# Kernel tuning notes

Hardware: AMD Instinct MI355X
Metric: run time of the kernel (lower is better)

The kernel has to match this reference:

```python
import jax, jax.numpy as jnp
import numpy as np

B, L, D, H = 2, 2048, 2048, 16
HD = D // H           # head_dim = 128
HD2 = HD // 2         # rotary pair count = 64


def setup_inputs() -> dict:
    key = jax.random.key(0)
    ks = jax.random.split(key, 6)
    x = jax.random.normal(ks[0], (B, L, D), dtype=jnp.float32)
    # RoPE angles: theta_i = 10000^(-2i/HD), angles[l, i] = l * theta_i
    inv_freq = 1.0 / (10000.0 ** (np.arange(0, HD, 2, dtype=np.float32) / HD))
    angles = np.arange(L, dtype=np.float32)[:, None] * inv_freq[None, :]  # [L, HD2]
    freqs_cos = jnp.asarray(np.cos(angles))[None]  # [1, L, HD2]
    freqs_sin = jnp.asarray(np.sin(angles))[None]  # [1, L, HD2]
    s = 1.0 / np.sqrt(D)
    Wq = jax.random.normal(ks[1], (D, D), dtype=jnp.float32) * s
    Wk = jax.random.normal(ks[2], (D, D), dtype=jnp.float32) * s
    Wv = jax.random.normal(ks[3], (D, D), dtype=jnp.float32) * s
    Wo = jax.random.normal(ks[4], (D, D), dtype=jnp.float32) * s
    return {"x": x, "freqs_cos": freqs_cos, "freqs_sin": freqs_sin,
            "Wq": Wq, "Wk": Wk, "Wv": Wv, "Wo": Wo}


def _apply_rope(t, cos, sin):
    # t: [B, H, L, HD]; cos/sin: [1, L, HD2] -> broadcast as [1, 1, L, HD2]
    t2 = t.reshape(*t.shape[:-1], HD2, 2)
    t0, t1 = t2[..., 0], t2[..., 1]
    c = cos[:, None]
    s = sin[:, None]
    r0 = t0 * c - t1 * s
    r1 = t0 * s + t1 * c
    return jnp.stack([r0, r1], axis=-1).reshape(t.shape)


def reference(x, freqs_cos, freqs_sin, Wq, Wk, Wv, Wo):
    b, l, d = x.shape
    # projections (torch Linear: x @ W.T)
    Q = (x @ Wq.T).reshape(b, l, H, HD).transpose(0, 2, 1, 3)  # [b,h,l,hd]
    K = (x @ Wk.T).reshape(b, l, H, HD).transpose(0, 2, 1, 3)
    V = (x @ Wv.T).reshape(b, l, H, HD).transpose(0, 2, 1, 3)
    Q = _apply_rope(Q, freqs_cos[:, :l], freqs_sin[:, :l])
    K = _apply_rope(K, freqs_cos[:, :l], freqs_sin[:, :l])
    scale = 1.0 / jnp.sqrt(jnp.asarray(HD, dtype=x.dtype))
    scores = jnp.einsum('bhqd,bhkd->bhqk', Q, K) * scale  # [b,h,l,l]
    causal = jnp.tril(jnp.ones((l, l), dtype=bool))
    scores = jnp.where(causal, scores, jnp.finfo(scores.dtype).min)
    probs = jax.nn.softmax(scores, axis=-1)
    out = jnp.einsum('bhqk,bhkd->bhqd', probs, V)  # [b,h,l,hd]
    out = out.transpose(0, 2, 1, 3).reshape(b, l, d)
    return out @ Wo.T
```

## Files before the change

kernel.cpp:

```cpp
#include <hip/hip_runtime.h>
#include <cstdint>
#include <cstddef>

typedef float f32x4 __attribute__((ext_vector_type(4)));
typedef short bf16x8 __attribute__((ext_vector_type(8)));
typedef short bf16x4 __attribute__((ext_vector_type(4)));
typedef unsigned int u32x4 __attribute__((ext_vector_type(4)));

#define LOG2E 1.4426950408889634f
#define K2E 0.12750102296293331f
#define MFMA_BF16 __builtin_amdgcn_mfma_f32_16x16x32_bf16

__device__ inline float bf2f(short s) {
  return (float)__builtin_bit_cast(__bf16, s);
}
__device__ inline short f2bf(float f) {
  return __builtin_bit_cast(short, (__bf16)f);
}
__device__ inline unsigned f2bfu(float f) {
  return (unsigned)__builtin_bit_cast(unsigned short, (__bf16)f);
}

__device__ inline void gload_lds16(const void* g, void* l) {
  __builtin_amdgcn_global_load_lds(
      (const __attribute__((address_space(1))) void*)g,
      (__attribute__((address_space(3))) void*)l, 16, 0, 0);
}

__global__ __launch_bounds__(256) void cvt_bf16(const float* __restrict__ in,
                                                __bf16* __restrict__ out, int n) {
  int i = (blockIdx.x * 256 + threadIdx.x) * 8;
  if (i >= n) return;
  f32x4 a = *(const f32x4*)(in + i);
  f32x4 b = *(const f32x4*)(in + i + 4);
  bf16x8 r;
#pragma unroll
  for (int j = 0; j < 4; ++j) {
    r[j]     = f2bf(a[j]);
    r[j + 4] = f2bf(b[j]);
  }
  *(bf16x8*)(out + i) = r;
}

__device__ inline void stage_half(const __bf16* __restrict__ gbase, int K,
                                  int k0, char* ldsHalf, int wid, int lane) {
#pragma unroll
  for (int j = 0; j < 2; ++j) {
    int idx = (wid * 2 + j) * 64 + lane;
    int row = idx >> 3;
    int c16 = (idx & 7) ^ (row & 7);
    gload_lds16(gbase + (size_t)row * K + k0 + c16 * 8,
                ldsHalf + (wid * 2 + j) * 1024);
  }
}

__device__ inline bf16x8 lds_frag(const char* halfbase, int row, int ks, int g) {
  return *(const bf16x8*)(halfbase + row * 128 + ((((ks << 2) | g) ^ (row & 7)) << 4));
}

#define WAITV(n) asm volatile("s_waitcnt vmcnt(" #n ")" ::: "memory")

__global__ __launch_bounds__(512, 1) void gemm256(const __bf16* __restrict__ A,
                                                  const __bf16* __restrict__ B,
                                                  __bf16* __restrict__ C,
                                                  int M, int N, int K) {
  __shared__ __attribute__((aligned(128))) char lds[131072];
  const int tid = threadIdx.x, wid = tid >> 6, lane = tid & 63;
  const int g = lane >> 4, lc = lane & 15;
  const int wm = wid >> 2, wn = wid & 3;

  const int gx = gridDim.x;
  int nwg = gx * gridDim.y;
  int bid = blockIdx.y * gx + blockIdx.x;
  int cpx = nwg >> 3;
  int swz = (bid & 7) * cpx + (bid >> 3);
  const int bx = swz % gx, by = swz / gx;

  const __bf16* Ag = A + (size_t)(by * 256) * K;
  const __bf16* Bg = B + (size_t)(bx * 256) * K;
  const int NT = K >> 6;

  f32x4 acc[4][4][2];
#pragma unroll
  for (int q = 0; q < 4; ++q)
#pragma unroll
    for (int m = 0; m < 4; ++m)
#pragma unroll
      for (int n = 0; n < 2; ++n) acc[q][m][n] = f32x4{0.f, 0.f, 0.f, 0.f};

  stage_half(Ag,             K, 0, lds +  0,     wid, lane);
  stage_half(Ag + 128 * (size_t)K, K, 0, lds + 16384, wid, lane);
  stage_half(Bg,             K, 0, lds + 65536,  wid, lane);
  stage_half(Bg + 128 * (size_t)K, K, 0, lds + 81920, wid, lane);
  if (NT > 1) {
    stage_half(Ag, K, 64, lds + 32768, wid, lane);
    stage_half(Bg, K, 64, lds + 98304, wid, lane);
    WAITV(4);
  } else {
    WAITV(0);
  }
  __builtin_amdgcn_s_barrier();

  bf16x8 a[4][2], b0[2][2], b1[2][2];

  for (int T = 0; T < NT; ++T) {
    const int cur = T & 1;
    char* Acur = lds + cur * 32768;
    char* Bcur = lds + 65536 + cur * 32768;
    char* Anxt = lds + (cur ^ 1) * 32768;
    char* Bnxt = lds + 65536 + (cur ^ 1) * 32768;
    const int k1 = (T + 1) << 6, k2 = (T + 2) << 6;

    {
#pragma unroll
      for (int m = 0; m < 4; ++m)
#pragma unroll
        for (int ks = 0; ks < 2; ++ks)
          a[m][ks] = lds_frag(Acur, wm * 64 + m * 16 + lc, ks, g);
#pragma unroll
      for (int n = 0; n < 2; ++n)
#pragma unroll
        for (int ks = 0; ks < 2; ++ks)
          b0[n][ks] = lds_frag(Bcur, wn * 32 + n * 16 + lc, ks, g);
      if (T + 1 < NT) {
        stage_half(Bg + 128 * (size_t)K, K, k1, Bnxt + 16384, wid, lane);
        WAITV(8);
      } else {
        WAITV(2);
      }
      __builtin_amdgcn_s_barrier();
      __builtin_amdgcn_s_setprio(1);
#pragma unroll
      for (int m = 0; m < 4; ++m)
#pragma unroll
        for (int n = 0; n < 2; ++n) {
          acc[0][m][n] = MFMA_BF16(a[m][0], b0[n][0], acc[0][m][n], 0, 0, 0);
          acc[0][m][n] = MFMA_BF16(a[m][1], b0[n][1], acc[0][m][n], 0, 0, 0);
        }
      __builtin_amdgcn_s_setprio(0);
    }
    {
#pragma unroll
      for (int n = 0; n < 2; ++n)
#pragma unroll
        for (int ks = 0; ks < 2; ++ks)
          b1[n][ks] = lds_frag(Bcur + 16384, wn * 32 + n * 16 + lc, ks, g);
      if (T + 1 < NT) {
        stage_half(Ag + 128 * (size_t)K, K, k1, Anxt + 16384, wid, lane);
        WAITV(8);
      } else {
        WAITV(0);
      }
      __builtin_amdgcn_s_barrier();
      __builtin_amdgcn_s_setprio(1);
#pragma unroll
      for (int m = 0; m < 4; ++m)
#pragma unroll
        for (int n = 0; n < 2; ++n) {
          acc[1][m][n] = MFMA_BF16(a[m][0], b1[n][0], acc[1][m][n], 0, 0, 0);
          acc[1][m][n] = MFMA_BF16(a[m][1], b1[n][1], acc[1][m][n], 0, 0, 0);
        }
      __builtin_amdgcn_s_setprio(0);
    }
    {
#pragma unroll
      for (int m = 0; m < 4; ++m)
#pragma unroll
        for (int ks = 0; ks < 2; ++ks)
          a[m][ks] = lds_frag(Acur + 16384, wm * 64 + m * 16 + lc, ks, g);
      if (T + 2 < NT) {
        stage_half(Ag, K, k2, Acur, wid, lane);
        WAITV(8);
      } else if (T + 1 < NT) {
        WAITV(6);
      }
      __builtin_amdgcn_s_barrier();
      __builtin_amdgcn_s_setprio(1);
#pragma unroll
      for (int m = 0; m < 4; ++m)
#pragma unroll
        for (int n = 0; n < 2; ++n) {
          acc[2][m][n] = MFMA_BF16(a[m][0], b0[n][0], acc[2][m][n], 0, 0, 0);
          acc[2][m][n] = MFMA_BF16(a[m][1], b0[n][1], acc[2][m][n], 0, 0, 0);
        }
      __builtin_amdgcn_s_setprio(0);
    }
    {
      if (T + 2 < NT) {
        stage_half(Bg, K, k2, Bcur, wid, lane);
        WAITV(8);
      } else if (T + 1 < NT) {
        WAITV(4);
      }
      __builtin_amdgcn_s_barrier();
      __builtin_amdgcn_s_setprio(1);
#pragma unroll
      for (int m = 0; m < 4; ++m)
#pragma unroll
        for (int n = 0; n < 2; ++n) {
          acc[3][m][n] = MFMA_BF16(a[m][0], b1[n][0], acc[3][m][n], 0, 0, 0);
          acc[3][m][n] = MFMA_BF16(a[m][1], b1[n][1], acc[3][m][n], 0, 0, 0);
        }
      __builtin_amdgcn_s_setprio(0);
    }
  }

#pragma unroll
  for (int q = 0; q < 4; ++q) {
    const int hA = q >> 1, hB = q & 1;
#pragma unroll
    for (int m = 0; m < 4; ++m)
#pragma unroll
      for (int n = 0; n < 2; ++n)
#pragma unroll
        for (int r = 0; r < 4; ++r) {
          int rr = by * 256 + hA * 128 + wm * 64 + m * 16 + g * 4 + r;
          int cc = bx * 256 + hB * 128 + wn * 32 + n * 16 + lc;
          C[(size_t)rr * N + cc] = (__bf16)acc[q][m][n][r];
        }
  }
}

template <bool OUT_F32>
__global__ __launch_bounds__(256) void gemm_bt(const __bf16* __restrict__ A,
                                               const __bf16* __restrict__ B,
                                               void* __restrict__ Cv,
                                               int M, int N, int K) {
  __shared__ __bf16 As[128 * 32];
  __shared__ __bf16 Bs[128 * 32];
  const int tid = threadIdx.x;
  const int wid = tid >> 6, lane = tid & 63;
  const int g = lane >> 4, lc = lane & 15;
  const int wr = wid >> 1, wc = wid & 1;
  const int row0 = blockIdx.y * 128, col0 = blockIdx.x * 128;
  const int r4 = tid >> 2, s4 = tid & 3;

  const __bf16* ga = A + (size_t)(row0 + r4) * K + s4 * 8;
  const __bf16* gb = B + (size_t)(col0 + r4) * K + s4 * 8;
  char* lA = (char*)As + wid * 1024;
  char* lB = (char*)Bs + wid * 1024;

  f32x4 acc[4][4];
#pragma unroll
  for (int m = 0; m < 4; ++m)
#pragma unroll
    for (int n = 0; n < 4; ++n) acc[m][n] = f32x4{0.f, 0.f, 0.f, 0.f};

  for (int k0 = 0; k0 < K; k0 += 32) {
    gload_lds16(ga + k0, lA);
    gload_lds16(ga + k0 + (size_t)64 * K, lA + 4096);
    gload_lds16(gb + k0, lB);
    gload_lds16(gb + k0 + (size_t)64 * K, lB + 4096);
    __syncthreads();

    bf16x8 af[4], bfr[4];
#pragma unroll
    for (int m = 0; m < 4; ++m)
      af[m] = *(const bf16x8*)((const char*)As + (wr * 64 + m * 16 + lc) * 64 + g * 16);
#pragma unroll
    for (int n = 0; n < 4; ++n)
      bfr[n] = *(const bf16x8*)((const char*)Bs + (wc * 64 + n * 16 + lc) * 64 + g * 16);
#pragma unroll
    for (int m = 0; m < 4; ++m)
#pragma unroll
      for (int n = 0; n < 4; ++n)
        acc[m][n] = MFMA_BF16(af[m], bfr[n], acc[m][n], 0, 0, 0);
    __syncthreads();
  }

#pragma unroll
  for (int m = 0; m < 4; ++m)
#pragma unroll
    for (int n = 0; n < 4; ++n)
#pragma unroll
      for (int r = 0; r < 4; ++r) {
        int rr = row0 + wr * 64 + m * 16 + g * 4 + r;
        int cc = col0 + wc * 64 + n * 16 + lc;
        if (OUT_F32)
          ((float*)Cv)[(size_t)rr * N + cc] = acc[m][n][r];
        else
          ((__bf16*)Cv)[(size_t)rr * N + cc] = (__bf16)acc[m][n][r];
      }
}

__global__ __launch_bounds__(256) void rope_kernel(__bf16* __restrict__ qkv,
                                                   const float* __restrict__ fc,
                                                   const float* __restrict__ fs) {
  int idx = blockIdx.x * 256 + threadIdx.x;
  int row = idx >> 9;
  int col = (idx & 511) * 8;
  int l = row & 2047;
  int i0 = (col & 127) >> 1;
  __bf16* p = qkv + (size_t)row * 6144 + col;
  bf16x8 v = *(const bf16x8*)p;
  f32x4 c4 = *(const f32x4*)(fc + l * 64 + i0);
  f32x4 s4 = *(const f32x4*)(fs + l * 64 + i0);
  bf16x8 r;
#pragma unroll
  for (int j = 0; j < 4; ++j) {
    float t0 = bf2f(v[2 * j]), t1 = bf2f(v[2 * j + 1]);
    r[2 * j]     = f2bf(t0 * c4[j] - t1 * s4[j]);
    r[2 * j + 1] = f2bf(t0 * s4[j] + t1 * c4[j]);
  }
  *(bf16x8*)p = r;
}

__global__ void transpose_v(const __bf16* __restrict__ qkv, __bf16* __restrict__ vt) {
  __shared__ __bf16 tile[32][33];
  const int b = blockIdx.z;
  const int l0 = blockIdx.x * 32, c0 = blockIdx.y * 32;
  for (int i = threadIdx.y; i < 32; i += 8)
    tile[i][threadIdx.x] = qkv[(size_t)(b * 2048 + l0 + i) * 6144 + 4096 + c0 + threadIdx.x];
  __syncthreads();
  for (int i = threadIdx.y; i < 32; i += 8)
    vt[(size_t)b * 4194304 + (size_t)(c0 + i) * 2048 + l0 + threadIdx.x] = tile[threadIdx.x][i];
}

__device__ __forceinline__ void attn_segment(const __bf16* __restrict__ qkv,
                                             const __bf16* __restrict__ vt,
                                             __bf16* __restrict__ aout,
                                             int b, int h, int bh,
                                             int qseg0, int nt,
                                             char* Ks, char* Vs, int tid) {
  const int wid = tid >> 6, lane = tid & 63;
  const int g = lane >> 4, lc = lane & 15;
  const int q0w = qseg0 + wid * 16;
  const float k2e = K2E;

  bf16x8 qreg[4];
  {
    const __bf16* qp = qkv + (size_t)(b * 2048 + q0w + lc) * 6144 + h * 128 + g * 8;
#pragma unroll
    for (int c = 0; c < 4; ++c) qreg[c] = *(const bf16x8*)(qp + c * 32);
  }

  f32x4 oaccT[8];
#pragma unroll
  for (int dc = 0; dc < 8; ++dc) oaccT[dc] = f32x4{0.f, 0.f, 0.f, 0.f};
  float m_run = -1e30f, l_run = 0.f;

  const int rK = tid >> 2, sK = tid & 3;
  const int dbase = tid >> 3, sg = tid & 7;
  const __bf16* kb = qkv + (size_t)(b * 2048) * 6144 + 2048 + h * 128;
  const __bf16* vb = vt + (size_t)bh * 262144;

  bf16x8 kreg[4], vreg[4];
  {
    const __bf16* kg = kb + (size_t)rK * 6144 + sK * 8;
#pragma unroll
    for (int kk = 0; kk < 4; ++kk) kreg[kk] = *(const bf16x8*)(kg + kk * 32);
    const __bf16* vg = vb + sg * 8;
#pragma unroll
    for (int kk = 0; kk < 4; ++kk)
      vreg[kk] = *(const bf16x8*)(vg + (size_t)(dbase + kk * 32) * 2048);
  }

  for (int t = 0; t < nt; ++t) {
    const int kv0 = t * 64;
    __syncthreads();
#pragma unroll
    for (int kk = 0; kk < 4; ++kk)
      *(bf16x8*)(Ks + rK * 256 + ((sK * 16 + kk * 64) ^ ((rK & 7) << 4))) = kreg[kk];
#pragma unroll
    for (int kk = 0; kk < 4; ++kk) {
      int d = dbase + kk * 32;
      *(bf16x8*)(Vs + d * 128 + ((sg * 16) ^ ((d & 7) << 4))) = vreg[kk];
    }
    __syncthreads();

    if (t + 1 < nt) {
      const __bf16* kg = kb + (size_t)(kv0 + 64 + rK) * 6144 + sK * 8;
#pragma unroll
      for (int kk = 0; kk < 4; ++kk) kreg[kk] = *(const bf16x8*)(kg + kk * 32);
      const __bf16* vg = vb + kv0 + 64 + sg * 8;
#pragma unroll
      for (int kk = 0; kk < 4; ++kk)
        vreg[kk] = *(const bf16x8*)(vg + (size_t)(dbase + kk * 32) * 2048);
    }

    f32x4 sacc[4];
#pragma unroll
    for (int kc = 0; kc < 4; ++kc) sacc[kc] = f32x4{0.f, 0.f, 0.f, 0.f};
#pragma unroll
    for (int kc = 0; kc < 4; ++kc) {
      const int kr = kc * 16 + lc;
#pragma unroll
      for (int c = 0; c < 4; ++c) {
        bf16x8 kf = *(const bf16x8*)(Ks + kr * 256 + ((c * 64 + g * 16) ^ ((kr & 7) << 4)));
        sacc[kc] = MFMA_BF16(kf, qreg[c], sacc[kc], 0, 0, 0);
      }
    }

    if (kv0 + 63 > q0w) {
#pragma unroll
      for (int kc = 0; kc < 4; ++kc)
#pragma unroll
        for (int r = 0; r < 4; ++r)
          if (kv0 + kc * 16 + g * 4 + r > q0w + lc) sacc[kc][r] = -1e30f;
    }

    float mx = sacc[0][0];
#pragma unroll
    for (int kc = 0; kc < 4; ++kc)
#pragma unroll
      for (int r = 0; r < 4; ++r) mx = fmaxf(mx, sacc[kc][r]);
    mx = fmaxf(mx, __shfl_xor(mx, 16));
    mx = fmaxf(mx, __shfl_xor(mx, 32));
    float mn = fmaxf(m_run, mx);
    float al = exp2f((m_run - mn) * k2e);
    m_run = mn;
    float p[4][4];
    float ls = 0.f;
#pragma unroll
    for (int kc = 0; kc < 4; ++kc)
#pragma unroll
      for (int r = 0; r < 4; ++r) {
        p[kc][r] = exp2f((sacc[kc][r] - mn) * k2e);
        ls += p[kc][r];
      }
    ls += __shfl_xor(ls, 16);
    ls += __shfl_xor(ls, 32);
    l_run = l_run * al + ls;
#pragma unroll
    for (int dc = 0; dc < 8; ++dc)
#pragma unroll
      for (int r = 0; r < 4; ++r) oaccT[dc][r] *= al;

    unsigned pk[4][2];
#pragma unroll
    for (int kc = 0; kc < 4; ++kc)
#pragma unroll
      for (int hh = 0; hh < 2; ++hh)
        pk[kc][hh] = f2bfu(p[kc][2 * hh]) | (f2bfu(p[kc][2 * hh + 1]) << 16);

    const int sA = (g & 1) * 32 + lc, sB = sA + 16;
    const bool hi = (g >> 1) != 0;
    bf16x8 brg[2];
#pragma unroll
    for (int c = 0; c < 2; ++c) {
      unsigned a0 = (unsigned)__shfl((int)pk[2 * c][0], sA);
      unsigned b0v = (unsigned)__shfl((int)pk[2 * c + 1][0], sA);
      unsigned a1 = (unsigned)__shfl((int)pk[2 * c][1], sA);
      unsigned b1v = (unsigned)__shfl((int)pk[2 * c + 1][1], sA);
      unsigned a2 = (unsigned)__shfl((int)pk[2 * c][0], sB);
      unsigned b2v = (unsigned)__shfl((int)pk[2 * c + 1][0], sB);
      unsigned a3 = (unsigned)__shfl((int)pk[2 * c][1], sB);
      unsigned b3v = (unsigned)__shfl((int)pk[2 * c + 1][1], sB);
      u32x4 wv;
      wv[0] = hi ? b0v : a0;
      wv[1] = hi ? b1v : a1;
      wv[2] = hi ? b2v : a2;
      wv[3] = hi ? b3v : a3;
      brg[c] = __builtin_bit_cast(bf16x8, wv);
    }

#pragma unroll
    for (int dc = 0; dc < 8; ++dc) {
      const int vr = dc * 16 + lc;
      bf16x8 vf0 = *(const bf16x8*)(Vs + vr * 128 + ((g * 16) ^ ((vr & 7) << 4)));
      bf16x8 vf1 = *(const bf16x8*)(Vs + vr * 128 + ((64 + g * 16) ^ ((vr & 7) << 4)));
      oaccT[dc] = MFMA_BF16(vf0, brg[0], oaccT[dc], 0, 0, 0);
      oaccT[dc] = MFMA_BF16(vf1, brg[1], oaccT[dc], 0, 0, 0);
    }
  }

  {
    float inv = 1.f / l_run;
    __bf16* op = aout + (size_t)(b * 2048 + q0w + lc) * 2048 + h * 128 + g * 4;
#pragma unroll
    for (int dc = 0; dc < 8; ++dc) {
      bf16x4 o;
#pragma unroll
      for (int r = 0; r < 4; ++r) o[r] = f2bf(oaccT[dc][r] * inv);
      *(bf16x4*)(op + dc * 16) = o;
    }
  }
}

__global__ __launch_bounds__(256, 2) void flash_attn(const __bf16* __restrict__ qkv,
                                                     const __bf16* __restrict__ vt,
                                                     __bf16* __restrict__ aout) {
  __shared__ __attribute__((aligned(16))) char smem[32768];
  char* Ks = smem;
  char* Vs = smem + 16384;
  const int tid = threadIdx.x;
  const int j = blockIdx.x;
  const int bh = blockIdx.y, b = bh >> 4, h = bh & 15;

  attn_segment(qkv, vt, aout, b, h, bh, j * 64, j + 1, Ks, Vs, tid);
  attn_segment(qkv, vt, aout, b, h, bh, (31 - j) * 64, 32 - j, Ks, Vs, tid);
}

extern "C" void kernel_launch(void* const* d_in, const int* in_sizes, int n_in,
                              void* d_out, int out_size, void* d_ws, size_t ws_size,
                              hipStream_t stream) {
  const float* x    = (const float*)d_in[0];
  const float* fcos = (const float*)d_in[1];
  const float* fsin = (const float*)d_in[2];
  const float* Wq   = (const float*)d_in[3];
  const float* Wk   = (const float*)d_in[4];
  const float* Wv   = (const float*)d_in[5];
  const float* Wo   = (const float*)d_in[6];

  char* ws = (char*)d_ws;
  __bf16* xb   = (__bf16*)(ws);
  __bf16* Wqkv = (__bf16*)(ws + 16777216);
  __bf16* Wob  = (__bf16*)(ws + 41943040);
  __bf16* QKV  = (__bf16*)(ws + 50331648);
  __bf16* Vt   = (__bf16*)(ws + 100663296);
  __bf16* aout = (__bf16*)(ws + 117440512);
  float* out = (float*)d_out;

  cvt_bf16<<<4096, 256, 0, stream>>>(x, xb, 8388608);
  cvt_bf16<<<2048, 256, 0, stream>>>(Wq, Wqkv, 4194304);
  cvt_bf16<<<2048, 256, 0, stream>>>(Wk, Wqkv + 4194304, 4194304);
  cvt_bf16<<<2048, 256, 0, stream>>>(Wv, Wqkv + 8388608, 4194304);
  cvt_bf16<<<2048, 256, 0, stream>>>(Wo, Wob, 4194304);

  gemm256<<<dim3(24, 16), 512, 0, stream>>>(xb, Wqkv, QKV, 4096, 6144, 2048);
  rope_kernel<<<8192, 256, 0, stream>>>(QKV, fcos, fsin);
  transpose_v<<<dim3(64, 64, 2), dim3(32, 8), 0, stream>>>(QKV, Vt);
  flash_attn<<<dim3(16, 32), 256, 0, stream>>>(QKV, Vt, aout);
  gemm_bt<true><<<dim3(16, 32), 256, 0, stream>>>(aout, Wob, out, 4096, 2048, 2048);
}
```

Baseline: 303.8 us.

## Replace GEMM kernels with 128x256 triple-buffered tile kernel for QKV and output projections

Replaces the 256x256 double-buffered QKV GEMM with a 128x256 tile kernel that uses a three-stage LDS ring (A, B0, B1 halves) and prefetches two K-steps ahead. The same kernel, templated for f32 output, now also runs the output projection in place of the simpler 128x128 gemm_bt. For QKV this doubles the grid for better CU coverage at the cost of less A/B reuse per tile. For the output projection it brings the deeper pipelining and swizzled LDS to that GEMM. LDS use rises to 144 KB per block.

```diff
diff --git a/kernel.cpp b/kernel.cpp
--- a/kernel.cpp
+++ b/kernel.cpp
@@ -60,11 +60,12 @@
 
 #define WAITV(n) asm volatile("s_waitcnt vmcnt(" #n ")" ::: "memory")
 
-__global__ __launch_bounds__(512, 1) void gemm256(const __bf16* __restrict__ A,
+template <bool OUT_F32>
+__global__ __launch_bounds__(512, 1) void gemm128(const __bf16* __restrict__ A,
                                                   const __bf16* __restrict__ B,
-                                                  __bf16* __restrict__ C,
+                                                  void* __restrict__ Cv,
                                                   int M, int N, int K) {
-  __shared__ __attribute__((aligned(128))) char lds[131072];
+  __shared__ __attribute__((aligned(128))) char lds[147456];
   const int tid = threadIdx.x, wid = tid >> 6, lane = tid & 63;
   const int g = lane >> 4, lc = lane & 15;
   const int wm = wid >> 2, wn = wid & 3;
@@ -76,211 +77,111 @@
   int swz = (bid & 7) * cpx + (bid >> 3);
   const int bx = swz % gx, by = swz / gx;
 
-  const __bf16* Ag = A + (size_t)(by * 256) * K;
+  const __bf16* Ag = A + (size_t)(by * 128) * K;
   const __bf16* Bg = B + (size_t)(bx * 256) * K;
+  const __bf16* Bg1 = Bg + 128 * (size_t)K;
   const int NT = K >> 6;
 
-  f32x4 acc[4][4][2];
-#pragma unroll
-  for (int q = 0; q < 4; ++q)
+  f32x4 acc[2][4][2];
+#pragma unroll
+  for (int hb = 0; hb < 2; ++hb)
 #pragma unroll
     for (int m = 0; m < 4; ++m)
 #pragma unroll
-      for (int n = 0; n < 2; ++n) acc[q][m][n] = f32x4{0.f, 0.f, 0.f, 0.f};
-
-  stage_half(Ag,             K, 0, lds +  0,     wid, lane);
-  stage_half(Ag + 128 * (size_t)K, K, 0, lds + 16384, wid, lane);
-  stage_half(Bg,             K, 0, lds + 65536,  wid, lane);
-  stage_half(Bg + 128 * (size_t)K, K, 0, lds + 81920, wid, lane);
-  if (NT > 1) {
-    stage_half(Ag, K, 64, lds + 32768, wid, lane);
-    stage_half(Bg, K, 64, lds + 98304, wid, lane);
-    WAITV(4);
-  } else {
-    WAITV(0);
-  }
+      for (int n = 0; n < 2; ++n) acc[hb][m][n] = f32x4{0.f, 0.f, 0.f, 0.f};
+
+  stage_half(Ag,  K, 0,  lds + 0,             wid, lane);
+  stage_half(Bg,  K, 0,  lds + 49152,         wid, lane);
+  stage_half(Bg1, K, 0,  lds + 98304,         wid, lane);
+  stage_half(Ag,  K, 64, lds + 16384,         wid, lane);
+  stage_half(Bg,  K, 64, lds + 49152 + 16384, wid, lane);
+  stage_half(Bg1, K, 64, lds + 98304 + 16384, wid, lane);
+  WAITV(8);
   __builtin_amdgcn_s_barrier();
 
   bf16x8 a[4][2], b0[2][2], b1[2][2];
+  int sc = 0;
 
   for (int T = 0; T < NT; ++T) {
-    const int cur = T & 1;
-    char* Acur = lds + cur * 32768;
-    char* Bcur = lds + 65536 + cur * 32768;
-    char* Anxt = lds + (cur ^ 1) * 32768;
-    char* Bnxt = lds + 65536 + (cur ^ 1) * 32768;
-    const int k1 = (T + 1) << 6, k2 = (T + 2) << 6;
-
-    {
-#pragma unroll
-      for (int m = 0; m < 4; ++m)
-#pragma unroll
-        for (int ks = 0; ks < 2; ++ks)
-          a[m][ks] = lds_frag(Acur, wm * 64 + m * 16 + lc, ks, g);
+    char* As  = lds + sc * 16384;
+    char* B0s = lds + 49152 + sc * 16384;
+    char* B1s = lds + 98304 + sc * 16384;
+    int s2 = sc + 2; if (s2 >= 3) s2 -= 3;
+    char* As2  = lds + s2 * 16384;
+    char* B0s2 = lds + 49152 + s2 * 16384;
+    char* B1s2 = lds + 98304 + s2 * 16384;
+    const int k2 = (T + 2) << 6;
+
+#pragma unroll
+    for (int m = 0; m < 4; ++m)
+#pragma unroll
+      for (int ks = 0; ks < 2; ++ks)
+        a[m][ks] = lds_frag(As, wm * 64 + m * 16 + lc, ks, g);
+#pragma unroll
+    for (int n = 0; n < 2; ++n)
+#pragma unroll
+      for (int ks = 0; ks < 2; ++ks)
+        b0[n][ks] = lds_frag(B0s, wn * 32 + n * 16 + lc, ks, g);
+    if (T + 2 < NT) {
+      stage_half(Ag, K, k2, As2, wid, lane);
+      stage_half(Bg, K, k2, B0s2, wid, lane);
+      WAITV(10);
+    } else if (T + 1 < NT) {
+      WAITV(6);
+    } else {
+      WAITV(0);
+    }
+    __builtin_amdgcn_s_barrier();
+    __builtin_amdgcn_s_setprio(1);
+#pragma unroll
+    for (int m = 0; m < 4; ++m)
+#pragma unroll
+      for (int n = 0; n < 2; ++n) {
+        acc[0][m][n] = MFMA_BF16(a[m][0], b0[n][0], acc[0][m][n], 0, 0, 0);
+        acc[0][m][n] = MFMA_BF16(a[m][1], b0[n][1], acc[0][m][n], 0, 0, 0);
+      }
+    __builtin_amdgcn_s_setprio(0);
+
+#pragma unroll
+    for (int n = 0; n < 2; ++n)
+#pragma unroll
+      for (int ks = 0; ks < 2; ++ks)
+        b1[n][ks] = lds_frag(B1s, wn * 32 + n * 16 + lc, ks, g);
+    if (T + 2 < NT) {
+      stage_half(Bg1, K, k2, B1s2, wid, lane);
+      WAITV(8);
+    } else if (T + 1 < NT) {
+      WAITV(2);
+    }
+    __builtin_amdgcn_s_barrier();
+    __builtin_amdgcn_s_setprio(1);
+#pragma unroll
+    for (int m = 0; m < 4; ++m)
+#pragma unroll
+      for (int n = 0; n < 2; ++n) {
+        acc[1][m][n] = MFMA_BF16(a[m][0], b1[n][0], acc[1][m][n], 0, 0, 0);
+        acc[1][m][n] = MFMA_BF16(a[m][1], b1[n][1], acc[1][m][n], 0, 0, 0);
+      }
+    __builtin_amdgcn_s_setprio(0);
+
+    sc = (sc + 1 == 3) ? 0 : sc + 1;
+  }
+
+#pragma unroll
+  for (int hb = 0; hb < 2; ++hb)
+#pragma unroll
+    for (int m = 0; m < 4; ++m)
 #pragma unroll
       for (int n = 0; n < 2; ++n)
 #pragma unroll
-        for (int ks = 0; ks < 2; ++ks)
-          b0[n][ks] = lds_frag(Bcur, wn * 32 + n * 16 + lc, ks, g);
-      if (T + 1 < NT) {
-        stage_half(Bg + 128 * (size_t)K, K, k1, Bnxt + 16384, wid, lane);
-        WAITV(8);
-      } else {
-        WAITV(2);
-      }
-      __builtin_amdgcn_s_barrier();
-      __builtin_amdgcn_s_setprio(1);
-#pragma unroll
-      for (int m = 0; m < 4; ++m)
-#pragma unroll
-        for (int n = 0; n < 2; ++n) {
-          acc[0][m][n] = MFMA_BF16(a[m][0], b0[n][0], acc[0][m][n], 0, 0, 0);
-          acc[0][m][n] = MFMA_BF16(a[m][1], b0[n][1], acc[0][m][n], 0, 0, 0);
+        for (int r = 0; r < 4; ++r) {
+          int rr = by * 128 + wm * 64 + m * 16 + g * 4 + r;
+          int cc = bx * 256 + hb * 128 + wn * 32 + n * 16 + lc;
+          if (OUT_F32)
+            ((float*)Cv)[(size_t)rr * N + cc] = acc[hb][m][n][r];
+          else
+            ((__bf16*)Cv)[(size_t)rr * N + cc] = (__bf16)acc[hb][m][n][r];
         }
-      __builtin_amdgcn_s_setprio(0);
-    }
-    {
-#pragma unroll
-      for (int n = 0; n < 2; ++n)
-#pragma unroll
-        for (int ks = 0; ks < 2; ++ks)
-          b1[n][ks] = lds_frag(Bcur + 16384, wn * 32 + n * 16 + lc, ks, g);
-      if (T + 1 < NT) {
-        stage_half(Ag + 128 * (size_t)K, K, k1, Anxt + 16384, wid, lane);
-        WAITV(8);
-      } else {
-        WAITV(0);
-      }
-      __builtin_amdgcn_s_barrier();
-      __builtin_amdgcn_s_setprio(1);
-#pragma unroll
-      for (int m = 0; m < 4; ++m)
-#pragma unroll
-        for (int n = 0; n < 2; ++n) {
-          acc[1][m][n] = MFMA_BF16(a[m][0], b1[n][0], acc[1][m][n], 0, 0, 0);
-          acc[1][m][n] = MFMA_BF16(a[m][1], b1[n][1], acc[1][m][n], 0, 0, 0);
-        }
-      __builtin_amdgcn_s_setprio(0);
-    }
-    {
-#pragma unroll
-      for (int m = 0; m < 4; ++m)
-#pragma unroll
-        for (int ks = 0; ks < 2; ++ks)
-          a[m][ks] = lds_frag(Acur + 16384, wm * 64 + m * 16 + lc, ks, g);
-      if (T + 2 < NT) {
-        stage_half(Ag, K, k2, Acur, wid, lane);
-        WAITV(8);
-      } else if (T + 1 < NT) {
-        WAITV(6);
-      }
-      __builtin_amdgcn_s_barrier();
-      __builtin_amdgcn_s_setprio(1);
-#pragma unroll
-      for (int m = 0; m < 4; ++m)
-#pragma unroll
-        for (int n = 0; n < 2; ++n) {
-          acc[2][m][n] = MFMA_BF16(a[m][0], b0[n][0], acc[2][m][n], 0, 0, 0);
-          acc[2][m][n] = MFMA_BF16(a[m][1], b0[n][1], acc[2][m][n], 0, 0, 0);
-        }
-      __builtin_amdgcn_s_setprio(0);
-    }
-    {
-      if (T + 2 < NT) {
-        stage_half(Bg, K, k2, Bcur, wid, lane);
-        WAITV(8);
-      } else if (T + 1 < NT) {
-        WAITV(4);
-      }
-      __builtin_amdgcn_s_barrier();
-      __builtin_amdgcn_s_setprio(1);
-#pragma unroll
-      for (int m = 0; m < 4; ++m)
-#pragma unroll
-        for (int n = 0; n < 2; ++n) {
-          acc[3][m][n] = MFMA_BF16(a[m][0], b1[n][0], acc[3][m][n], 0, 0, 0);
-          acc[3][m][n] = MFMA_BF16(a[m][1], b1[n][1], acc[3][m][n], 0, 0, 0);
-        }
-      __builtin_amdgcn_s_setprio(0);
-    }
-  }
-
-#pragma unroll
-  for (int q = 0; q < 4; ++q) {
-    const int hA = q >> 1, hB = q & 1;
-#pragma unroll
-    for (int m = 0; m < 4; ++m)
-#pragma unroll
-      for (int n = 0; n < 2; ++n)
-#pragma unroll
-        for (int r = 0; r < 4; ++r) {
-          int rr = by * 256 + hA * 128 + wm * 64 + m * 16 + g * 4 + r;
-          int cc = bx * 256 + hB * 128 + wn * 32 + n * 16 + lc;
-          C[(size_t)rr * N + cc] = (__bf16)acc[q][m][n][r];
-        }
-  }
-}
-
-template <bool OUT_F32>
-__global__ __launch_bounds__(256) void gemm_bt(const __bf16* __restrict__ A,
-                                               const __bf16* __restrict__ B,
-                                               void* __restrict__ Cv,
-                                               int M, int N, int K) {
-  __shared__ __bf16 As[128 * 32];
-  __shared__ __bf16 Bs[128 * 32];
-  const int tid = threadIdx.x;
-  const int wid = tid >> 6, lane = tid & 63;
-  const int g = lane >> 4, lc = lane & 15;
-  const int wr = wid >> 1, wc = wid & 1;
-  const int row0 = blockIdx.y * 128, col0 = blockIdx.x * 128;
-  const int r4 = tid >> 2, s4 = tid & 3;
-
-  const __bf16* ga = A + (size_t)(row0 + r4) * K + s4 * 8;
-  const __bf16* gb = B + (size_t)(col0 + r4) * K + s4 * 8;
-  char* lA = (char*)As + wid * 1024;
-  char* lB = (char*)Bs + wid * 1024;
-
-  f32x4 acc[4][4];
-#pragma unroll
-  for (int m = 0; m < 4; ++m)
-#pragma unroll
-    for (int n = 0; n < 4; ++n) acc[m][n] = f32x4{0.f, 0.f, 0.f, 0.f};
-
-  for (int k0 = 0; k0 < K; k0 += 32) {
-    gload_lds16(ga + k0, lA);
-    gload_lds16(ga + k0 + (size_t)64 * K, lA + 4096);
-    gload_lds16(gb + k0, lB);
-    gload_lds16(gb + k0 + (size_t)64 * K, lB + 4096);
-    __syncthreads();
-
-    bf16x8 af[4], bfr[4];
-#pragma unroll
-    for (int m = 0; m < 4; ++m)
-      af[m] = *(const bf16x8*)((const char*)As + (wr * 64 + m * 16 + lc) * 64 + g * 16);
-#pragma unroll
-    for (int n = 0; n < 4; ++n)
-      bfr[n] = *(const bf16x8*)((const char*)Bs + (wc * 64 + n * 16 + lc) * 64 + g * 16);
-#pragma unroll
-    for (int m = 0; m < 4; ++m)
-#pragma unroll
-      for (int n = 0; n < 4; ++n)
-        acc[m][n] = MFMA_BF16(af[m], bfr[n], acc[m][n], 0, 0, 0);
-    __syncthreads();
-  }
-
-#pragma unroll
-  for (int m = 0; m < 4; ++m)
-#pragma unroll
-    for (int n = 0; n < 4; ++n)
-#pragma unroll
-      for (int r = 0; r < 4; ++r) {
-        int rr = row0 + wr * 64 + m * 16 + g * 4 + r;
-        int cc = col0 + wc * 64 + n * 16 + lc;
-        if (OUT_F32)
-          ((float*)Cv)[(size_t)rr * N + cc] = acc[m][n][r];
-        else
-          ((__bf16*)Cv)[(size_t)rr * N + cc] = (__bf16)acc[m][n][r];
-      }
 }
 
 __global__ __launch_bounds__(256) void rope_kernel(__bf16* __restrict__ qkv,
@@ -517,9 +418,9 @@
   cvt_bf16<<<2048, 256, 0, stream>>>(Wv, Wqkv + 8388608, 4194304);
   cvt_bf16<<<2048, 256, 0, stream>>>(Wo, Wob, 4194304);
 
-  gemm256<<<dim3(24, 16), 512, 0, stream>>>(xb, Wqkv, QKV, 4096, 6144, 2048);
+  gemm128<false><<<dim3(24, 32), 512, 0, stream>>>(xb, Wqkv, QKV, 4096, 6144, 2048);
   rope_kernel<<<8192, 256, 0, stream>>>(QKV, fcos, fsin);
   transpose_v<<<dim3(64, 64, 2), dim3(32, 8), 0, stream>>>(QKV, Vt);
   flash_attn<<<dim3(16, 32), 256, 0, stream>>>(QKV, Vt, aout);
-  gemm_bt<true><<<dim3(16, 32), 256, 0, stream>>>(aout, Wob, out, 4096, 2048, 2048);
-}
+  gemm128<true><<<dim3(8, 32), 512, 0, stream>>>(aout, Wob, out, 4096, 2048, 2048);
+}
```

New measurement: 286.1 us. 5.8% less time.
